# Kernel optimization log

Hardware: AMD Instinct MI355X
Metric: run time of the kernel (lower is better)

The kernel has to match this reference:

```python
import jax, jax.numpy as jnp
import numpy as np

B, S, T = 4, 4096, 512
D_MODEL, D_TEXT = 1024, 768
H, KVH, HD = 16, 2, 64  # heads, kv heads, head_dim; rep = H // KVH
REP = H // KVH
EPS = 1e-5


def setup_inputs() -> dict:
    key = jax.random.key(0)
    k = jax.random.split(key, 6)
    std = 0.02
    return {
        "x": jax.random.normal(k[0], (B, S, D_MODEL), jnp.float32),
        "text_input": jax.random.normal(k[1], (B, T, D_TEXT), jnp.float32),
        "ln_w": jnp.ones((D_TEXT,), jnp.float32),
        "ln_b": jnp.zeros((D_TEXT,), jnp.float32),
        # weights stored as [in, out] (transposed torch Linear layout)
        "Wq": jax.random.normal(k[2], (D_MODEL, D_MODEL), jnp.float32) * std,
        "Wkv": jax.random.normal(k[3], (D_TEXT, 2 * KVH * HD), jnp.float32) * std,
        "Wout": jax.random.normal(k[4], (D_MODEL, D_MODEL), jnp.float32) * std,
        "bout": jnp.zeros((D_MODEL,), jnp.float32),
    }


def reference(x, text_input, ln_w, ln_b, Wq, Wkv, Wout, bout):
    # LayerNorm over d_text
    mu = jnp.mean(text_input, axis=-1, keepdims=True)
    var = jnp.var(text_input, axis=-1, keepdims=True)
    tn = (text_input - mu) * jax.lax.rsqrt(var + EPS) * ln_w + ln_b

    # Projections
    Q = (x @ Wq).reshape(B, S, KVH, REP, HD)          # heads are kv-major: h = g*REP + r
    KV = tn @ Wkv                                      # [B, T, 2*KVH*HD]
    K, V = jnp.split(KV, 2, axis=-1)
    K = K.reshape(B, T, KVH, HD)
    V = V.reshape(B, T, KVH, HD)

    # Grouped-query attention without materializing repeated K/V
    scale = 1.0 / np.sqrt(HD)
    scores = jnp.einsum('bsgrd,btgd->bgrst', Q, K) * scale  # [B,KVH,REP,S,T]
    attn = jax.nn.softmax(scores, axis=-1)
    O = jnp.einsum('bgrst,btgd->bsgrd', attn, V).reshape(B, S, D_MODEL)

    return O @ Wout + bout
```

## Files before the change

### kernel.cpp

```cpp
#include <hip/hip_runtime.h>
#include <hip/hip_bf16.h>


#define B_    4
#define S_    4096
#define T_    512
#define DM_   1024
#define DT_   768
#define H_    16
#define KVH_  2
#define HD_   64

#define GLOBAL_AS __attribute__((address_space(1)))
#define LDS_AS    __attribute__((address_space(3)))

typedef __bf16 bf16x8 __attribute__((ext_vector_type(8)));
typedef float  f32x4  __attribute__((ext_vector_type(4)));

__global__ __launch_bounds__(256) void cast_f32_bf16(const float* __restrict__ in,
                                                     __hip_bfloat16* __restrict__ out) {
    int i = blockIdx.x * 256 + threadIdx.x;
    float4 v = ((const float4*)in)[i];
    union { ushort4 u; __hip_bfloat16 h[4]; } p;
    p.h[0] = __float2bfloat16(v.x);
    p.h[1] = __float2bfloat16(v.y);
    p.h[2] = __float2bfloat16(v.z);
    p.h[3] = __float2bfloat16(v.w);
    ((ushort4*)out)[i] = p.u;
}

__global__ __launch_bounds__(256) void transpose_cast(const float* __restrict__ in,
                                                      __hip_bfloat16* __restrict__ out,
                                                      int R, int C) {
    __shared__ float tile[32][33];
    int tx = threadIdx.x, ty = threadIdx.y;
    int r0 = blockIdx.y * 32, c0 = blockIdx.x * 32;
#pragma unroll
    for (int k = 0; k < 4; k++)
        tile[ty + 8 * k][tx] = in[(size_t)(r0 + ty + 8 * k) * C + c0 + tx];
    __syncthreads();
#pragma unroll
    for (int k = 0; k < 4; k++)
        out[(size_t)(c0 + ty + 8 * k) * R + r0 + tx] = __float2bfloat16(tile[tx][ty + 8 * k]);
}

__global__ __launch_bounds__(256) void ln_kv_kernel(const float* __restrict__ text,
                                                    const float* __restrict__ lnw,
                                                    const float* __restrict__ lnb,
                                                    const float* __restrict__ Wkv,
                                                    __hip_bfloat16* __restrict__ Kg,
                                                    __hip_bfloat16* __restrict__ Vt) {
    __shared__ float tn[8][DT_];
    __shared__ float red[2][256];
    int tid = threadIdx.x;
    int b  = blockIdx.x >> 6;
    int t0 = (blockIdx.x & 63) * 8;

    for (int j = 0; j < 8; j++) {
        const float* row = text + (size_t)(b * T_ + t0 + j) * DT_;
        float v0 = row[tid], v1 = row[tid + 256], v2 = row[tid + 512];
        red[0][tid] = v0 + v1 + v2;
        red[1][tid] = v0 * v0 + v1 * v1 + v2 * v2;
        __syncthreads();
        for (int ofs = 128; ofs > 0; ofs >>= 1) {
            if (tid < ofs) { red[0][tid] += red[0][tid + ofs]; red[1][tid] += red[1][tid + ofs]; }
            __syncthreads();
        }
        float mu  = red[0][0] * (1.0f / DT_);
        float var = red[1][0] * (1.0f / DT_) - mu * mu;
        float rs  = rsqrtf(var + 1e-5f);
        tn[j][tid]       = (v0 - mu) * rs * lnw[tid]       + lnb[tid];
        tn[j][tid + 256] = (v1 - mu) * rs * lnw[tid + 256] + lnb[tid + 256];
        tn[j][tid + 512] = (v2 - mu) * rs * lnw[tid + 512] + lnb[tid + 512];
        __syncthreads();
    }

    float acc[8] = {0, 0, 0, 0, 0, 0, 0, 0};
    for (int k = 0; k < DT_; k++) {
        float w = Wkv[(size_t)k * 256 + tid];
#pragma unroll
        for (int j = 0; j < 8; j++) acc[j] += tn[j][k] * w;
    }
    int c = tid;
    int isV = c >> 7;
    int cc = c & 127, g = cc >> 6, d = cc & 63;
#pragma unroll
    for (int j = 0; j < 8; j++) {
        int t = t0 + j;
        __hip_bfloat16 hv = __float2bfloat16(acc[j]);
        if (!isV) Kg[((size_t)(b * KVH_ + g) * T_ + t) * HD_ + d] = hv;
        else      Vt[((size_t)(b * KVH_ + g) * HD_ + d) * T_ + t] = hv;
    }
}

template <int EPI>
__global__ __launch_bounds__(256) void gemm_bt(const __hip_bfloat16* __restrict__ A,
                                               const __hip_bfloat16* __restrict__ Bt,
                                               void* __restrict__ Cout,
                                               const float* __restrict__ bias,
                                               float scale, int M, int N, int K) {
    __shared__ __bf16 As[128 * 32];
    __shared__ __bf16 Bs[128 * 32];
    int tid = threadIdx.x;
    int w = tid >> 6, lane = tid & 63, q = lane >> 4, cL = lane & 15;
    int wm = (w >> 1) * 64, wn = (w & 1) * 64;
    size_t m0 = (size_t)blockIdx.y * 128, n0 = (size_t)blockIdx.x * 128;
    const __bf16* Ab = (const __bf16*)A;
    const __bf16* Bb = (const __bf16*)Bt;
    f32x4 acc[4][4] = {};

    int row_s[2], ko_s[2];
#pragma unroll
    for (int it = 0; it < 2; it++) {
        int id = tid + it * 256;
        int sr = id >> 3, U = (id & 7) ^ (sr & 7);
        row_s[it] = 2 * sr + (U >> 2);
        ko_s[it]  = (U & 3) * 8;
    }
    int offA[4], offB[4];
#pragma unroll
    for (int i = 0; i < 4; i++) {
        int Ra = wm + 16 * i + cL;
        offA[i] = (Ra >> 1) * 64 + ((((Ra & 1) * 4 + q) ^ ((Ra >> 1) & 7)) * 8);
        int Rb = wn + 16 * i + cL;
        offB[i] = (Rb >> 1) * 64 + ((((Rb & 1) * 4 + q) ^ ((Rb >> 1) & 7)) * 8);
    }

    for (int k0 = 0; k0 < K; k0 += 32) {
#pragma unroll
        for (int it = 0; it < 2; it++) {
            int id = tid + it * 256;
            __builtin_amdgcn_global_load_lds(
                (const GLOBAL_AS void*)(Ab + (m0 + row_s[it]) * K + k0 + ko_s[it]),
                (LDS_AS void*)(&As[id * 8]), 16, 0, 0);
            __builtin_amdgcn_global_load_lds(
                (const GLOBAL_AS void*)(Bb + (n0 + row_s[it]) * K + k0 + ko_s[it]),
                (LDS_AS void*)(&Bs[id * 8]), 16, 0, 0);
        }
        __syncthreads();
        bf16x8 af[4], bf[4];
#pragma unroll
        for (int i = 0; i < 4; i++) af[i] = *(const bf16x8*)&As[offA[i]];
#pragma unroll
        for (int j = 0; j < 4; j++) bf[j] = *(const bf16x8*)&Bs[offB[j]];
#pragma unroll
        for (int i = 0; i < 4; i++)
#pragma unroll
            for (int j = 0; j < 4; j++)
                acc[i][j] = __builtin_amdgcn_mfma_f32_16x16x32_bf16(af[i], bf[j], acc[i][j], 0, 0, 0);
        __syncthreads();
    }

#pragma unroll
    for (int i = 0; i < 4; i++)
#pragma unroll
        for (int j = 0; j < 4; j++) {
            size_t r   = m0 + wm + 16 * i + 4 * q;
            size_t col = n0 + wn + 16 * j + cL;
#pragma unroll
            for (int ii = 0; ii < 4; ii++) {
                float v = acc[i][j][ii];
                if (EPI == 0)
                    ((__hip_bfloat16*)Cout)[(r + ii) * N + col] = __float2bfloat16(v * scale);
                else
                    ((float*)Cout)[(r + ii) * N + col] = v + bias[col];
            }
        }
}

__global__ __launch_bounds__(256, 4) void attn_kernel(const __hip_bfloat16* __restrict__ Qs,
                                                      const __hip_bfloat16* __restrict__ Kg,
                                                      const __hip_bfloat16* __restrict__ Vt,
                                                      __hip_bfloat16* __restrict__ Oc) {
    __shared__ __bf16 Ks[64 * 64];
    __shared__ __bf16 Vs[64 * 64];
    __shared__ __bf16 Ps[4][1024];
    int tid = threadIdx.x;
    int w = tid >> 6, lane = tid & 63, q = lane >> 4, cL = lane & 15;
    int bh = blockIdx.y;
    int b = bh >> 4, h = bh & 15, g = h >> 3;
    int s0 = blockIdx.x * 128 + w * 32;

    const __bf16* Qb = (const __bf16*)Qs;
    const __bf16* Kb = (const __bf16*)Kg + (size_t)(b * KVH_ + g) * T_ * HD_;
    const __bf16* Vb = (const __bf16*)Vt + (size_t)(b * KVH_ + g) * HD_ * T_;
    __bf16* pw = &Ps[w][0];

    int ksoff[2], vsoff[2];
#pragma unroll
    for (int it = 0; it < 2; it++) {
        int U = tid + it * 256;
        int r = U >> 3, us = (U & 7) ^ (r & 7);
        ksoff[it] = r * HD_ + us * 8;
        vsoff[it] = r * T_  + us * 8;
    }

    bf16x8 aq[2][2];
#pragma unroll
    for (int mi = 0; mi < 2; mi++) {
        size_t base = ((size_t)(b * S_) + s0 + mi * 16 + cL) * DM_ + h * HD_ + 8 * q;
        aq[mi][0] = *(const bf16x8*)(Qb + base);
        aq[mi][1] = *(const bf16x8*)(Qb + base + 32);
    }

    float lpart[2][4] = {};
    f32x4 oacc[2][4] = {};

#pragma unroll 1
    for (int tc = 0; tc < 8; tc++) {
        int t0 = tc * 64;
#pragma unroll
        for (int it = 0; it < 2; it++) {
            int U = tid + it * 256;
            __builtin_amdgcn_global_load_lds(
                (const GLOBAL_AS void*)(Kb + (size_t)t0 * HD_ + ksoff[it]),
                (LDS_AS void*)(&Ks[U * 8]), 16, 0, 0);
            __builtin_amdgcn_global_load_lds(
                (const GLOBAL_AS void*)(Vb + t0 + vsoff[it]),
                (LDS_AS void*)(&Vs[U * 8]), 16, 0, 0);
        }
        __syncthreads();

        f32x4 sc[2][4];
#pragma unroll
        for (int nt = 0; nt < 4; nt++) {
            int R = 16 * nt + cL;
            bf16x8 k0 = *(const bf16x8*)&Ks[R * 64 + ((q ^ (R & 7)) * 8)];
            bf16x8 k1 = *(const bf16x8*)&Ks[R * 64 + (((4 + q) ^ (R & 7)) * 8)];
#pragma unroll
            for (int mi = 0; mi < 2; mi++) {
                f32x4 a = {0.f, 0.f, 0.f, 0.f};
                a = __builtin_amdgcn_mfma_f32_16x16x32_bf16(aq[mi][0], k0, a, 0, 0, 0);
                a = __builtin_amdgcn_mfma_f32_16x16x32_bf16(aq[mi][1], k1, a, 0, 0, 0);
                sc[mi][nt] = a;
            }
        }

#pragma unroll
        for (int mi = 0; mi < 2; mi++)
#pragma unroll
            for (int i = 0; i < 4; i++) {
                float ls = 0.f;
#pragma unroll
                for (int nt = 0; nt < 4; nt++) {
                    float e = __expf(sc[mi][nt][i]); sc[mi][nt][i] = e; ls += e;
                }
                lpart[mi][i] += ls;
            }

#pragma unroll
        for (int ksc = 0; ksc < 2; ksc++) {
#pragma unroll
            for (int mi = 0; mi < 2; mi++)
#pragma unroll
                for (int half = 0; half < 2; half++) {
                    int nt = 2 * ksc + half;
                    int tin = half * 16 + cL;
                    int off = mi * 512 + (((tin >> 3) * 16 + 4 * q) * 8) + (tin & 7);
#pragma unroll
                    for (int i = 0; i < 4; i++)
                        pw[off + i * 8] = (__bf16)sc[mi][nt][i];
                }
            bf16x8 pa0 = *(const bf16x8*)&pw[lane * 8];
            bf16x8 pa1 = *(const bf16x8*)&pw[512 + lane * 8];
#pragma unroll
            for (int nd = 0; nd < 4; nd++) {
                int D = 16 * nd + cL;
                bf16x8 bv = *(const bf16x8*)&Vs[D * 64 + (((4 * ksc + q) ^ (D & 7)) * 8)];
                oacc[0][nd] = __builtin_amdgcn_mfma_f32_16x16x32_bf16(pa0, bv, oacc[0][nd], 0, 0, 0);
                oacc[1][nd] = __builtin_amdgcn_mfma_f32_16x16x32_bf16(pa1, bv, oacc[1][nd], 0, 0, 0);
            }
        }
        __syncthreads();
    }

#pragma unroll
    for (int mi = 0; mi < 2; mi++) {
        float rinv[4];
#pragma unroll
        for (int i = 0; i < 4; i++) {
            float l = lpart[mi][i];
            l += __shfl_xor(l, 1); l += __shfl_xor(l, 2);
            l += __shfl_xor(l, 4); l += __shfl_xor(l, 8);
            rinv[i] = 1.0f / l;
        }
#pragma unroll
        for (int nd = 0; nd < 4; nd++)
#pragma unroll
            for (int i = 0; i < 4; i++) {
                float v = oacc[mi][nd][i] * rinv[i];
                size_t s = (size_t)(b * S_) + s0 + mi * 16 + 4 * q + i;
                Oc[s * DM_ + h * HD_ + nd * 16 + cL] = __float2bfloat16(v);
            }
    }
}

extern "C" void kernel_launch(void* const* d_in, const int* in_sizes, int n_in,
                              void* d_out, int out_size, void* d_ws, size_t ws_size,
                              hipStream_t stream) {
    const float* x    = (const float*)d_in[0];
    const float* text = (const float*)d_in[1];
    const float* lnw  = (const float*)d_in[2];
    const float* lnb  = (const float*)d_in[3];
    const float* Wq   = (const float*)d_in[4];
    const float* Wkv  = (const float*)d_in[5];
    const float* Wout = (const float*)d_in[6];
    const float* bout = (const float*)d_in[7];

    char* ws = (char*)d_ws;
    __hip_bfloat16* xbf = (__hip_bfloat16*)(ws);
    __hip_bfloat16* Qs  = (__hip_bfloat16*)(ws + 33554432);
    __hip_bfloat16* Wqt = (__hip_bfloat16*)(ws + 67108864);
    __hip_bfloat16* Wot = (__hip_bfloat16*)(ws + 69206016);
    __hip_bfloat16* Kg  = (__hip_bfloat16*)(ws + 71303168);
    __hip_bfloat16* Vtp = (__hip_bfloat16*)(ws + 71827456);

    cast_f32_bf16<<<dim3((B_ * S_ * DM_) / 4 / 256), dim3(256), 0, stream>>>(x, xbf);
    transpose_cast<<<dim3(32, 32), dim3(32, 8), 0, stream>>>(Wq, Wqt, DM_, DM_);
    transpose_cast<<<dim3(32, 32), dim3(32, 8), 0, stream>>>(Wout, Wot, DM_, DM_);
    ln_kv_kernel<<<dim3(B_ * T_ / 8), dim3(256), 0, stream>>>(text, lnw, lnb, Wkv, Kg, Vtp);

    gemm_bt<0><<<dim3(DM_ / 128, (B_ * S_) / 128), dim3(256), 0, stream>>>(
        xbf, Wqt, (void*)Qs, nullptr, 0.125f, B_ * S_, DM_, DM_);

    attn_kernel<<<dim3(S_ / 128, B_ * H_), dim3(256), 0, stream>>>(Qs, Kg, Vtp, xbf);

    gemm_bt<1><<<dim3(DM_ / 128, (B_ * S_) / 128), dim3(256), 0, stream>>>(
        xbf, Wot, d_out, bout, 1.0f, B_ * S_, DM_, DM_);
}
```

Baseline: 368.2 us.

## Replace 128x128 GEMM with 256x256 double-buffered pipelined MFMA kernel

Replaces the projection GEMMs with a 512-thread kernel computing 256x256 output tiles over 64-wide K steps. LDS is double-buffered so global_load_lds prefetches of the next tiles overlap the MFMA work, interleaved across four phases with setprio and waitcnt control. The aim is more data reuse per LDS load and less stall on memory and barriers. It costs 128 KB of LDS per block, which limits occupancy to one block per CU, and it fixes a single wave of 256 blocks.

```diff
diff --git a/kernel.cpp b/kernel.cpp
--- a/kernel.cpp
+++ b/kernel.cpp
@@ -94,78 +94,118 @@
 }
 
 template <int EPI>
-__global__ __launch_bounds__(256) void gemm_bt(const __hip_bfloat16* __restrict__ A,
-                                               const __hip_bfloat16* __restrict__ Bt,
-                                               void* __restrict__ Cout,
-                                               const float* __restrict__ bias,
-                                               float scale, int M, int N, int K) {
-    __shared__ __bf16 As[128 * 32];
-    __shared__ __bf16 Bs[128 * 32];
-    int tid = threadIdx.x;
-    int w = tid >> 6, lane = tid & 63, q = lane >> 4, cL = lane & 15;
-    int wm = (w >> 1) * 64, wn = (w & 1) * 64;
-    size_t m0 = (size_t)blockIdx.y * 128, n0 = (size_t)blockIdx.x * 128;
-    const __bf16* Ab = (const __bf16*)A;
-    const __bf16* Bb = (const __bf16*)Bt;
-    f32x4 acc[4][4] = {};
-
-    int row_s[2], ko_s[2];
-#pragma unroll
-    for (int it = 0; it < 2; it++) {
-        int id = tid + it * 256;
-        int sr = id >> 3, U = (id & 7) ^ (sr & 7);
-        row_s[it] = 2 * sr + (U >> 2);
-        ko_s[it]  = (U & 3) * 8;
-    }
-    int offA[4], offB[4];
-#pragma unroll
-    for (int i = 0; i < 4; i++) {
-        int Ra = wm + 16 * i + cL;
-        offA[i] = (Ra >> 1) * 64 + ((((Ra & 1) * 4 + q) ^ ((Ra >> 1) & 7)) * 8);
-        int Rb = wn + 16 * i + cL;
-        offB[i] = (Rb >> 1) * 64 + ((((Rb & 1) * 4 + q) ^ ((Rb >> 1) & 7)) * 8);
-    }
-
-    for (int k0 = 0; k0 < K; k0 += 32) {
-#pragma unroll
-        for (int it = 0; it < 2; it++) {
-            int id = tid + it * 256;
+__global__ __launch_bounds__(512, 2) void gemm256(const __hip_bfloat16* __restrict__ A,
+                                                  const __hip_bfloat16* __restrict__ Bt,
+                                                  void* __restrict__ Cout,
+                                                  const float* __restrict__ bias,
+                                                  float scale, int M, int N, int K) {
+    __shared__ __bf16 lds[65536];
+    const int tid = threadIdx.x;
+    const int w = tid >> 6, lane = tid & 63, q = lane >> 4, cL = lane & 15;
+    const int wm = w >> 2, wn = w & 3;
+    const size_t m0 = (size_t)blockIdx.y * 256, n0 = (size_t)blockIdx.x * 256;
+    const __bf16* Ab = (const __bf16*)A + m0 * K;
+    const __bf16* Bb = (const __bf16*)Bt + n0 * K;
+    const int NT = K >> 6;
+
+    int srcoff[2], dstoff[2];
+#pragma unroll
+    for (int it = 0; it < 2; ++it) {
+        int id = tid + it * 512;
+        int r = id >> 3, u = (id & 7) ^ (r & 7);
+        srcoff[it] = r * K + u * 8;
+        dstoff[it] = id * 8;
+    }
+
+    const int swz0 = ((0 + q) ^ (cL & 7)) * 8;
+    const int swz1 = ((4 + q) ^ (cL & 7)) * 8;
+    const int baseA = (wm * 128 + cL) * 64;
+    const int baseB = (wn * 64 + cL) * 64;
+
+    f32x4 acc[8][4] = {};
+
+    auto STAGE = [&](int isB, int j, int tt) {
+        const __bf16* g = (isB ? Bb : Ab) + (size_t)j * 128 * K + (size_t)tt * 64;
+        const int sb = (tt & 1) * 32768 + isB * 16384 + j * 8192;
+#pragma unroll
+        for (int it = 0; it < 2; ++it)
             __builtin_amdgcn_global_load_lds(
-                (const GLOBAL_AS void*)(Ab + (m0 + row_s[it]) * K + k0 + ko_s[it]),
-                (LDS_AS void*)(&As[id * 8]), 16, 0, 0);
-            __builtin_amdgcn_global_load_lds(
-                (const GLOBAL_AS void*)(Bb + (n0 + row_s[it]) * K + k0 + ko_s[it]),
-                (LDS_AS void*)(&Bs[id * 8]), 16, 0, 0);
-        }
-        __syncthreads();
-        bf16x8 af[4], bf[4];
-#pragma unroll
-        for (int i = 0; i < 4; i++) af[i] = *(const bf16x8*)&As[offA[i]];
-#pragma unroll
-        for (int j = 0; j < 4; j++) bf[j] = *(const bf16x8*)&Bs[offB[j]];
-#pragma unroll
-        for (int i = 0; i < 4; i++)
-#pragma unroll
-            for (int j = 0; j < 4; j++)
-                acc[i][j] = __builtin_amdgcn_mfma_f32_16x16x32_bf16(af[i], bf[j], acc[i][j], 0, 0, 0);
-        __syncthreads();
-    }
-
-#pragma unroll
-    for (int i = 0; i < 4; i++)
-#pragma unroll
-        for (int j = 0; j < 4; j++) {
-            size_t r   = m0 + wm + 16 * i + 4 * q;
-            size_t col = n0 + wn + 16 * j + cL;
-#pragma unroll
-            for (int ii = 0; ii < 4; ii++) {
-                float v = acc[i][j][ii];
+                (const GLOBAL_AS void*)(g + srcoff[it]),
+                (LDS_AS void*)(&lds[sb + dstoff[it]]), 16, 0, 0);
+    };
+
+    STAGE(0, 0, 0); STAGE(0, 1, 0); STAGE(1, 0, 0); STAGE(1, 1, 0);
+    if (NT > 1) { STAGE(0, 0, 1); STAGE(0, 1, 1); }
+    asm volatile("s_waitcnt vmcnt(4)" ::: "memory");
+    __builtin_amdgcn_s_barrier();
+    __builtin_amdgcn_sched_barrier(0);
+
+    for (int t = 0; t < NT; ++t) {
+        const int sb = (t & 1) * 32768;
+        const __bf16* As = lds + sb;
+        const __bf16* Bs = lds + sb + 16384;
+        bf16x8 af[4][2];
+#pragma unroll
+        for (int ph = 0; ph < 4; ++ph) {
+            const int mh = ph >> 1, nh = ph & 1;
+            if (nh == 0) {
+#pragma unroll
+                for (int m = 0; m < 4; ++m) {
+                    int ro = baseA + mh * 4096 + m * 1024;
+                    af[m][0] = *(const bf16x8*)&As[ro + swz0];
+                    af[m][1] = *(const bf16x8*)&As[ro + swz1];
+                }
+            }
+            bf16x8 bq[2][2];
+#pragma unroll
+            for (int n = 0; n < 2; ++n) {
+                int ro = baseB + nh * 2048 + n * 1024;
+                bq[n][0] = *(const bf16x8*)&Bs[ro + swz0];
+                bq[n][1] = *(const bf16x8*)&Bs[ro + swz1];
+            }
+            if (ph == 0)      { if (t + 1 < NT) STAGE(1, 0, t + 1); }
+            else if (ph == 1) { if (t + 1 < NT) STAGE(1, 1, t + 1); }
+            else if (ph == 3 && t + 2 < NT) { STAGE(0, 0, t + 2); STAGE(0, 1, t + 2); }
+
+            __builtin_amdgcn_s_barrier();
+            __builtin_amdgcn_sched_barrier(0);
+            __builtin_amdgcn_s_setprio(1);
+#pragma unroll
+            for (int m = 0; m < 4; ++m)
+#pragma unroll
+                for (int n = 0; n < 2; ++n) {
+                    f32x4* a = &acc[mh * 4 + m][nh * 2 + n];
+                    *a = __builtin_amdgcn_mfma_f32_16x16x32_bf16(af[m][0], bq[n][0], *a, 0, 0, 0);
+                    *a = __builtin_amdgcn_mfma_f32_16x16x32_bf16(af[m][1], bq[n][1], *a, 0, 0, 0);
+                }
+            __builtin_amdgcn_s_setprio(0);
+            if (ph == 3) {
+                if (t + 2 < NT)      asm volatile("s_waitcnt vmcnt(4)" ::: "memory");
+                else if (t + 1 < NT) asm volatile("s_waitcnt vmcnt(0)" ::: "memory");
+            }
+            __builtin_amdgcn_s_barrier();
+            __builtin_amdgcn_sched_barrier(0);
+        }
+    }
+
+#pragma unroll
+    for (int jn = 0; jn < 4; ++jn) {
+        size_t col = n0 + wn * 64 + jn * 16 + cL;
+        float bb = 0.0f;
+        if (EPI == 1) bb = bias[col];
+#pragma unroll
+        for (int im = 0; im < 8; ++im) {
+            size_t r = m0 + wm * 128 + im * 16 + 4 * q;
+#pragma unroll
+            for (int ii = 0; ii < 4; ++ii) {
+                float v = acc[im][jn][ii];
                 if (EPI == 0)
                     ((__hip_bfloat16*)Cout)[(r + ii) * N + col] = __float2bfloat16(v * scale);
                 else
-                    ((float*)Cout)[(r + ii) * N + col] = v + bias[col];
-            }
-        }
+                    ((float*)Cout)[(r + ii) * N + col] = v + bb;
+            }
+        }
+    }
 }
 
 __global__ __launch_bounds__(256, 4) void attn_kernel(const __hip_bfloat16* __restrict__ Qs,
@@ -320,11 +360,11 @@
     transpose_cast<<<dim3(32, 32), dim3(32, 8), 0, stream>>>(Wout, Wot, DM_, DM_);
     ln_kv_kernel<<<dim3(B_ * T_ / 8), dim3(256), 0, stream>>>(text, lnw, lnb, Wkv, Kg, Vtp);
 
-    gemm_bt<0><<<dim3(DM_ / 128, (B_ * S_) / 128), dim3(256), 0, stream>>>(
+    gemm256<0><<<dim3(DM_ / 256, (B_ * S_) / 256), dim3(512), 0, stream>>>(
         xbf, Wqt, (void*)Qs, nullptr, 0.125f, B_ * S_, DM_, DM_);
 
     attn_kernel<<<dim3(S_ / 128, B_ * H_), dim3(256), 0, stream>>>(Qs, Kg, Vtp, xbf);
 
-    gemm_bt<1><<<dim3(DM_ / 128, (B_ * S_) / 128), dim3(256), 0, stream>>>(
+    gemm256<1><<<dim3(DM_ / 256, (B_ * S_) / 256), dim3(512), 0, stream>>>(
         xbf, Wot, d_out, bout, 1.0f, B_ * S_, DM_, DM_);
 }
```

Result: faster. 341.6 us (-7.2%).
